# Kernel tuning notes

Hardware: AMD Instinct MI355X
Metric: run time of the kernel (lower is better)

Reference implementation:

```python
import jax, jax.numpy as jnp
import numpy as np

B, D, C, F = 1024, 8192, 345, 512
PROTO_W = 0.99  # args.proto_m


def setup_inputs() -> dict:
    key = jax.random.key(0)
    k = jax.random.split(key, 6)
    img_q = jax.random.normal(k[0], (B, D), jnp.float32)
    img_q1 = jax.random.normal(k[1], (B, D), jnp.float32)
    # partial label mask: random candidate set, guarantee >=1 candidate per row
    partial_Y = (jax.random.uniform(k[2], (B, C)) < 0.3).astype(jnp.float32)
    partial_Y = partial_Y.at[jnp.arange(B), jnp.arange(B) % C].set(1.0)
    W_enc = jax.random.normal(k[3], (D, F), jnp.float32) / np.sqrt(D).astype(np.float32)
    W_fc = jax.random.normal(k[4], (F, C), jnp.float32) / np.sqrt(F).astype(np.float32)
    b_fc = jnp.zeros((C,), jnp.float32)
    proto = jax.random.normal(k[5], (C, F), jnp.float32)
    proto = proto / jnp.linalg.norm(proto, axis=1, keepdims=True)
    return {"img_q": img_q, "img_q1": img_q1, "partial_Y": partial_Y,
            "W_enc": W_enc, "W_fc": W_fc, "b_fc": b_fc, "proto": proto}


def reference(img_q, img_q1, partial_Y, W_enc, W_fc, b_fc, proto):
    # encoder: feats [B,F], logits [B,C] (abstracted backbone + shared fc)
    feats_q = img_q @ W_enc
    logits_q = feats_q @ W_fc + b_fc
    feats_q1 = img_q1 @ W_enc
    logits_q1 = feats_q1 @ W_fc + b_fc

    # partial-label restricted pseudo labels
    scores = jax.nn.softmax(logits_q, axis=1) * partial_Y
    scores = scores / scores.sum(axis=1, keepdims=True)
    labels = jnp.argmax(scores, axis=1)  # [B] int

    # Sequential per-sample EMA p[l] = w*p[l] + (1-w)*f, vectorized in closed form.
    # For a sample with c_after same-label samples occurring later, its final
    # contribution is (1-w)*w^c_after * f; the old prototype is scaled by w^count.
    onehot = jax.nn.one_hot(labels, C, dtype=feats_q.dtype)   # [B,C]
    cum = jnp.cumsum(onehot, axis=0)                          # inclusive counts
    occ = cum[jnp.arange(B), labels] - 1.0                    # occurrences before i
    total = cum[-1]                                           # [C] per-class counts
    c_after = total[labels] - occ - 1.0                       # [B]
    coef = (1.0 - PROTO_W) * PROTO_W ** c_after               # [B]
    contrib = jax.ops.segment_sum(coef[:, None] * feats_q, labels, num_segments=C)
    new_proto = (PROTO_W ** total)[:, None] * proto + contrib
    new_proto = new_proto / jnp.linalg.norm(new_proto, axis=1, keepdims=True)

    prot_scores = new_proto @ W_fc + b_fc
    return logits_q, logits_q1, new_proto, prot_scores, labels, feats_q, feats_q1
```

## Files before the change

### kernel.cpp

```cpp
#include <hip/hip_runtime.h>
#include <float.h>
#include <math.h>

#define B_SZ 1024
#define D_SZ 8192
#define C_SZ 345
#define F_SZ 512
#define PROTO_W 0.99f


#define WS_XH 0
#define WS_XL 33554432u
#define WS_WH 67108864u
#define WS_WL 75497472u
#define WS_P  83886080u
#define WS2_WFH 100663296u
#define WS2_WFL 101056512u
#define WS2_LAB 101449728u
#define WS2_NEED 101457920u
#define WS2_FH 0u
#define WS2_FL 2097152u

#define WS_NEED 92274688u
#define WS_FH  0u
#define WS_FL  2097152u
#define WS_WFH 4194304u
#define WS_WFL 4587520u
#define WS_NPH 4980736u
#define WS_NPL 5373952u

typedef short bf16x8 __attribute__((ext_vector_type(8)));
typedef short short4v __attribute__((ext_vector_type(4)));
typedef short short8v __attribute__((ext_vector_type(8)));
typedef float f32x4  __attribute__((ext_vector_type(4)));

__device__ __forceinline__ void split_bf16(float x, short& hi, short& lo) {
    unsigned u = __float_as_uint(x);
    unsigned r = (u + 0x7FFFu + ((u >> 16) & 1u)) >> 16;
    hi = (short)r;
    float hf = __uint_as_float(r << 16);
    lo = (short)(__float_as_uint(x - hf) >> 16);
}
__device__ __forceinline__ float bf16_f32(short h) {
    return __uint_as_float(((unsigned)(unsigned short)h) << 16);
}

__device__ __forceinline__ void gl_lds16(const short* g, short* l) {
    __builtin_amdgcn_global_load_lds(
        (const __attribute__((address_space(1))) void*)g,
        (__attribute__((address_space(3))) void*)l, 16, 0, 0);
}

__device__ __forceinline__ unsigned f2key(float v) {
    unsigned u = __float_as_uint(v);
    return (u & 0x80000000u) ? ~u : (u | 0x80000000u);
}

__device__ __forceinline__ void fence_barrier() {
    asm volatile("" ::: "memory");
    __builtin_amdgcn_s_barrier();
    asm volatile("" ::: "memory");
}

#define MFMA_BF16 __builtin_amdgcn_mfma_f32_16x16x32_bf16

#define MFMA_BLOCK(IA0, IA1, IB0, IB1)                                   \
    do {                                                                 \
        bf16x8 a0h = *(const bf16x8*)&sAh[IA0];                          \
        bf16x8 a1h = *(const bf16x8*)&sAh[IA1];                          \
        bf16x8 b0h = *(const bf16x8*)&sBh[IB0];                          \
        bf16x8 b1h = *(const bf16x8*)&sBh[IB1];                          \
        bf16x8 a0l = *(const bf16x8*)&sAl[IA0];                          \
        bf16x8 a1l = *(const bf16x8*)&sAl[IA1];                          \
        bf16x8 b0l = *(const bf16x8*)&sBl[IB0];                          \
        bf16x8 b1l = *(const bf16x8*)&sBl[IB1];                          \
        acc[0][0] = MFMA_BF16(a0h, b0h, acc[0][0], 0, 0, 0);             \
        acc[0][1] = MFMA_BF16(a0h, b1h, acc[0][1], 0, 0, 0);             \
        acc[1][0] = MFMA_BF16(a1h, b0h, acc[1][0], 0, 0, 0);             \
        acc[1][1] = MFMA_BF16(a1h, b1h, acc[1][1], 0, 0, 0);             \
        acc[0][0] = MFMA_BF16(a0h, b0l, acc[0][0], 0, 0, 0);             \
        acc[0][1] = MFMA_BF16(a0h, b1l, acc[0][1], 0, 0, 0);             \
        acc[1][0] = MFMA_BF16(a1h, b0l, acc[1][0], 0, 0, 0);             \
        acc[1][1] = MFMA_BF16(a1h, b1l, acc[1][1], 0, 0, 0);             \
        acc[0][0] = MFMA_BF16(a0l, b0h, acc[0][0], 0, 0, 0);             \
        acc[0][1] = MFMA_BF16(a0l, b1h, acc[0][1], 0, 0, 0);             \
        acc[1][0] = MFMA_BF16(a1l, b0h, acc[1][0], 0, 0, 0);             \
        acc[1][1] = MFMA_BF16(a1l, b1h, acc[1][1], 0, 0, 0);             \
    } while (0)

__global__ __launch_bounds__(256) void convert_all(
    const float* __restrict__ img_q, const float* __restrict__ img_q1,
    const float* __restrict__ W_enc, const float* __restrict__ W_fc,
    short* __restrict__ Xh, short* __restrict__ Xl,
    short* __restrict__ Wh, short* __restrict__ Wl,
    short* __restrict__ Wth, short* __restrict__ Wtl)
{
    __shared__ float tile[64][65];
    const int bid = blockIdx.x;
    const int t = threadIdx.x;

    if (bid < 1024) {
        const int HALF = (B_SZ * D_SZ) / 4;
        const int total = 2 * HALF;
        for (int i4 = bid * 256 + t; i4 < total; i4 += 1024 * 256) {
            float4 v = (i4 < HALF) ? ((const float4*)img_q)[i4]
                                   : ((const float4*)img_q1)[i4 - HALF];
            short4v h, l;
            short hh, ll;
            split_bf16(v.x, hh, ll); h.x = hh; l.x = ll;
            split_bf16(v.y, hh, ll); h.y = hh; l.y = ll;
            split_bf16(v.z, hh, ll); h.z = hh; l.z = ll;
            split_bf16(v.w, hh, ll); h.w = hh; l.w = ll;
            ((short4v*)Xh)[i4] = h;
            ((short4v*)Xl)[i4] = l;
        }
    } else if (bid < 2048) {
        const int id = bid - 1024;
        const int k0 = (id >> 3) * 64;
        const int n0 = (id & 7) * 64;
        {
            const int kr = t >> 2;
            const int cb = (t & 3) * 16;
#pragma unroll
            for (int j = 0; j < 4; ++j) {
                float4 v = *(const float4*)&W_enc[(size_t)(k0 + kr) * F_SZ + n0 + cb + j * 4];
                tile[kr][cb + j * 4 + 0] = v.x;
                tile[kr][cb + j * 4 + 1] = v.y;
                tile[kr][cb + j * 4 + 2] = v.z;
                tile[kr][cb + j * 4 + 3] = v.w;
            }
        }
        __syncthreads();
        const int n = t >> 2;
#pragma unroll
        for (int cc = 0; cc < 2; ++cc) {
            const int ch = (t & 3) * 2 + cc;
            short8v h, l;
#pragma unroll
            for (int e = 0; e < 8; ++e) {
                short hh, ll;
                split_bf16(tile[ch * 8 + e][n], hh, ll);
                h[e] = hh; l[e] = ll;
            }
            size_t off = (size_t)(n0 + n) * D_SZ + k0 + ch * 8;
            *(short8v*)&Wh[off] = h;
            *(short8v*)&Wl[off] = l;
        }
    } else {
        const int id = bid - 2048;
        const int k0 = (id & 7) * 64;
        const int c0 = (id >> 3) * 64;
        for (int idx = t; idx < 64 * 64; idx += 256) {
            const int kr = idx >> 6;
            const int cc = idx & 63;
            tile[kr][cc] = (c0 + cc < C_SZ) ? W_fc[(size_t)(k0 + kr) * C_SZ + c0 + cc] : 0.0f;
        }
        __syncthreads();
        const int crow = t >> 2;
#pragma unroll
        for (int cc2 = 0; cc2 < 2; ++cc2) {
            const int ch = (t & 3) * 2 + cc2;
            short8v h, l;
#pragma unroll
            for (int e = 0; e < 8; ++e) {
                short hh, ll;
                split_bf16(tile[ch * 8 + e][crow], hh, ll);
                h[e] = hh; l[e] = ll;
            }
            size_t off = (size_t)(c0 + crow) * F_SZ + k0 + ch * 8;
            *(short8v*)&Wth[off] = h;
            *(short8v*)&Wtl[off] = l;
        }
    }
}

__global__ __launch_bounds__(256, 1) void gemm_ws128(
    const short* __restrict__ Xh, const short* __restrict__ Xl,
    const short* __restrict__ Wh, const short* __restrict__ Wl,
    float* __restrict__ P, int ksteps)
{
    __shared__ __align__(16) short sAh[2][8192];
    __shared__ __align__(16) short sAl[2][8192];
    __shared__ __align__(16) short sBh[2][8192];
    __shared__ __align__(16) short sBl[2][8192];

    const int t = threadIdx.x;
    const int lane = t & 63;
    const int wave = t >> 6;
    const int nt = blockIdx.x;
    const int mt = blockIdx.y;
    const int ks = blockIdx.z;
    const int m0 = mt * 128;
    const int n0 = nt * 128;
    const int kbase = ks * ksteps * 64;

    const short* gbase =
        (wave == 0) ? Xh + (size_t)m0 * D_SZ :
        (wave == 1) ? Xl + (size_t)m0 * D_SZ :
        (wave == 2) ? Wh + (size_t)n0 * D_SZ :
                      Wl + (size_t)n0 * D_SZ;
    short* lb[2];
    lb[0] = (wave == 0) ? sAh[0] : (wave == 1) ? sAl[0] : (wave == 2) ? sBh[0] : sBl[0];
    lb[1] = (wave == 0) ? sAh[1] : (wave == 1) ? sAl[1] : (wave == 2) ? sBh[1] : sBl[1];
    const int lrow8 = lane >> 3;
    const int gchunkOff = ((lane & 7) ^ lrow8) * 8;
    const short* gsrc = gbase + (size_t)lrow8 * D_SZ + kbase + gchunkOff;

    const int mo = (wave >> 1) * 64;
    const int no = (wave & 1) * 64;
    const int lr = lane & 15;
    const int lkg = lane >> 4;
    const int x7 = lr & 7;
    const int sl0 = lkg ^ x7;
    const int sl1 = (4 + lkg) ^ x7;
    int aoff[4], boff[4];
#pragma unroll
    for (int f = 0; f < 4; ++f) {
        aoff[f] = (mo + 16 * f + lr) * 64;
        boff[f] = (no + 16 * f + lr) * 64;
    }

    f32x4 acc[4][4] = {};

#pragma unroll
    for (int j = 0; j < 16; ++j)
        gl_lds16(gsrc + (size_t)(8 * j) * D_SZ, lb[0] + j * 512);

    int buf = 0;
    for (int s = 0; s < ksteps; ++s) {
        if (s + 1 < ksteps) {
            short* dst = lb[buf ^ 1];
            const short* g = gsrc + (s + 1) * 64;
#pragma unroll
            for (int j = 0; j < 16; ++j)
                gl_lds16(g + (size_t)(8 * j) * D_SZ, dst + j * 512);
            asm volatile("s_waitcnt vmcnt(16)" ::: "memory");
        } else {
            asm volatile("s_waitcnt vmcnt(0)" ::: "memory");
        }
        fence_barrier();

        __builtin_amdgcn_s_setprio(1);
        {
            const short* pAh = sAh[buf];
            const short* pAl = sAl[buf];
            const short* pBh = sBh[buf];
            const short* pBl = sBl[buf];
#pragma unroll
            for (int ksub = 0; ksub < 2; ++ksub) {
                const int sl = ksub ? sl1 : sl0;
                bf16x8 ah[4], al[4], bh[4], blo[4];
#pragma unroll
                for (int f = 0; f < 4; ++f) {
                    ah[f]  = *(const bf16x8*)&pAh[aoff[f] + sl * 8];
                    al[f]  = *(const bf16x8*)&pAl[aoff[f] + sl * 8];
                }
#pragma unroll
                for (int g = 0; g < 4; ++g) {
                    bh[g]  = *(const bf16x8*)&pBh[boff[g] + sl * 8];
                    blo[g] = *(const bf16x8*)&pBl[boff[g] + sl * 8];
                }
#pragma unroll
                for (int f = 0; f < 4; ++f)
#pragma unroll
                    for (int g = 0; g < 4; ++g)
                        acc[f][g] = MFMA_BF16(ah[f], bh[g], acc[f][g], 0, 0, 0);
#pragma unroll
                for (int f = 0; f < 4; ++f)
#pragma unroll
                    for (int g = 0; g < 4; ++g)
                        acc[f][g] = MFMA_BF16(ah[f], blo[g], acc[f][g], 0, 0, 0);
#pragma unroll
                for (int f = 0; f < 4; ++f)
#pragma unroll
                    for (int g = 0; g < 4; ++g)
                        acc[f][g] = MFMA_BF16(al[f], bh[g], acc[f][g], 0, 0, 0);
            }
        }
        __builtin_amdgcn_s_setprio(0);
        fence_barrier();
        buf ^= 1;
    }

    float* Pout = P + (size_t)ks * (2048u * 512u);
#pragma unroll
    for (int f = 0; f < 4; ++f)
#pragma unroll
        for (int g = 0; g < 4; ++g) {
            const int col  = n0 + no + 16 * g + (lane & 15);
            const int row0 = m0 + mo + 16 * f + (lane >> 4) * 4;
#pragma unroll
            for (int r = 0; r < 4; ++r)
                Pout[(size_t)(row0 + r) * F_SZ + col] = acc[f][g][r];
        }
}

__global__ __launch_bounds__(256) void reduce_feats4(
    const float* __restrict__ P, float* __restrict__ feats,
    short* __restrict__ Fh, short* __restrict__ Fl)
{
    const int i4 = blockIdx.x * 256 + threadIdx.x;
    float4 a = ((const float4*)P)[i4];
#pragma unroll
    for (int sl = 1; sl < 4; ++sl) {
        float4 b = ((const float4*)(P + (size_t)sl * (2048u * 512u)))[i4];
        a.x += b.x; a.y += b.y; a.z += b.z; a.w += b.w;
    }
    ((float4*)feats)[i4] = a;
    float v[4] = {a.x, a.y, a.z, a.w};
    short4v h, l;
    short hh, ll;
#pragma unroll
    for (int e = 0; e < 4; ++e) {
        split_bf16(v[e], hh, ll); h[e] = hh; l[e] = ll;
    }
    ((short4v*)Fh)[i4] = h;
    ((short4v*)Fl)[i4] = l;
}

__global__ __launch_bounds__(256, 2) void fc_logits3(
    const short* __restrict__ Ah, const short* __restrict__ Al,
    const short* __restrict__ Bh_g, const short* __restrict__ Bl_g,
    const float* __restrict__ bias, const float* __restrict__ partial_Y,
    float* __restrict__ logits, unsigned long long* __restrict__ labPack)
{
    __shared__ __align__(16) short dAh[2][4096];
    __shared__ __align__(16) short dAl[2][4096];
    __shared__ __align__(16) short dBh[2][4096];
    __shared__ __align__(16) short dBl[2][4096];

    const int t = threadIdx.x;
    const int lane = t & 63;
    const int wave = t >> 6;
    const int n0 = blockIdx.x * 64;
    const int m0 = blockIdx.y * 64;

    const int lrow8 = lane >> 3;
    const int colOff = ((lane & 7) ^ lrow8) * 8;

    const short* gsrc = (wave == 0) ? Ah : (wave == 1) ? Al
                      : (wave == 2) ? Bh_g : Bl_g;
    const int rbase = (wave < 2) ? m0 : n0;
    short* lb[2];
    lb[0] = (wave == 0) ? dAh[0] : (wave == 1) ? dAl[0] : (wave == 2) ? dBh[0] : dBl[0];
    lb[1] = (wave == 0) ? dAh[1] : (wave == 1) ? dAl[1] : (wave == 2) ? dBh[1] : dBl[1];
    const short* gbase = gsrc + (size_t)(rbase + lrow8) * F_SZ + colOff;

    const int mo = (wave >> 1) * 32;
    const int no = (wave & 1) * 32;
    const int lr = lane & 15;
    const int lkg = lane >> 4;
    const int x7 = lr & 7;
    const int sl0 = (0 + lkg) ^ x7;
    const int sl1 = (4 + lkg) ^ x7;
    const int ra0 = (mo + lr) * 64,      ra1 = (mo + 16 + lr) * 64;
    const int rb0 = (no + lr) * 64,      rb1 = (no + 16 + lr) * 64;
    const int a00 = ra0 + sl0 * 8, a01 = ra0 + sl1 * 8;
    const int a10 = ra1 + sl0 * 8, a11 = ra1 + sl1 * 8;
    const int b00 = rb0 + sl0 * 8, b01 = rb0 + sl1 * 8;
    const int b10 = rb1 + sl0 * 8, b11 = rb1 + sl1 * 8;

    f32x4 acc[2][2] = {};

#pragma unroll
    for (int j = 0; j < 8; ++j)
        gl_lds16(gbase + (size_t)(8 * j) * F_SZ, lb[0] + j * 512);

    int buf = 0;
    for (int s = 0; s < 8; ++s) {
        if (s + 1 < 8) {
            short* dst = lb[buf ^ 1];
            const short* g = gbase + (s + 1) * 64;
#pragma unroll
            for (int j = 0; j < 8; ++j)
                gl_lds16(g + (size_t)(8 * j) * F_SZ, dst + j * 512);
            asm volatile("s_waitcnt vmcnt(8)" ::: "memory");
        } else {
            asm volatile("s_waitcnt vmcnt(0)" ::: "memory");
        }
        fence_barrier();
        __builtin_amdgcn_s_setprio(1);
        {
            const short* sAh = dAh[buf];
            const short* sAl = dAl[buf];
            const short* sBh = dBh[buf];
            const short* sBl = dBl[buf];
            MFMA_BLOCK(a00, a10, b00, b10);
            MFMA_BLOCK(a01, a11, b01, b11);
        }
        __builtin_amdgcn_s_setprio(0);
        fence_barrier();
        buf ^= 1;
    }

    const bool doArg = (m0 < B_SZ);
#pragma unroll
    for (int f = 0; f < 2; ++f) {
#pragma unroll
        for (int r = 0; r < 4; ++r) {
            const int row = m0 + mo + f * 16 + (lane >> 4) * 4 + r;
            unsigned long long best = 0;
#pragma unroll
            for (int g = 0; g < 2; ++g) {
                const int col = n0 + no + g * 16 + (lane & 15);
                if (col < C_SZ) {
                    const float v = acc[f][g][r] + bias[col];
                    logits[(size_t)row * C_SZ + col] = v;
                    if (doArg && partial_Y[(size_t)row * C_SZ + col] != 0.0f) {
                        unsigned long long p = ((unsigned long long)f2key(v) << 32)
                                             | (unsigned long long)(0xFFFFFFFFu - (unsigned)col);
                        if (p > best) best = p;
                    }
                }
            }
            if (doArg) {
#pragma unroll
                for (int m = 1; m < 16; m <<= 1) {
                    unsigned long long o = __shfl_xor(best, m);
                    if (o > best) best = o;
                }
                if ((lane & 15) == 0 && best != 0)
                    atomicMax(&labPack[row], best);
            }
        }
    }
}

__global__ __launch_bounds__(512) void proto_scores_fused(
    const unsigned long long* __restrict__ labPack,
    const float* __restrict__ feats_q,
    const float* __restrict__ proto,
    const short* __restrict__ Wth, const short* __restrict__ Wtl,
    const float* __restrict__ b_fc,
    float* __restrict__ new_proto, float* __restrict__ scores,
    float* __restrict__ labels_f)
{
    __shared__ int rowlist[B_SZ];
    __shared__ int mcount_s;
    __shared__ float nprow[F_SZ];
    __shared__ float red[8];
    __shared__ float rinv_s;
    const int c = blockIdx.x;
    const int t = threadIdx.x;
    const int lane = t & 63;
    const int w = t >> 6;

    if (c == 0) {
#pragma unroll
        for (int j = 0; j < 2; ++j) {
            const int i = t + j * 512;
            int li = (int)(0xFFFFFFFFu - (unsigned)(labPack[i] & 0xFFFFFFFFull));
            labels_f[i] = (float)li;
        }
    }

    if (w == 0) {
        int k = 0;
#pragma unroll
        for (int ch = 0; ch < 16; ++ch) {
            unsigned long long pk = labPack[ch * 64 + lane];
            int li = (int)(0xFFFFFFFFu - (unsigned)(pk & 0xFFFFFFFFull));
            unsigned long long mask = __ballot(li == c);
            if (lane == 0) {
                while (mask) {
                    int p = __builtin_ctzll(mask);
                    mask &= mask - 1;
                    rowlist[k++] = ch * 64 + p;
                }
            }
            k = __shfl(k, 0);
        }
        if (lane == 0) mcount_s = k;
    }
    __syncthreads();
    const int m = mcount_s;

    float val = proto[(size_t)c * F_SZ + t];
    for (int k = 0; k < m; ++k)
        val = PROTO_W * val + (1.0f - PROTO_W) * feats_q[(size_t)rowlist[k] * F_SZ + t];

    float sq = val * val;
#pragma unroll
    for (int off = 32; off; off >>= 1) sq += __shfl_down(sq, off);
    if ((t & 63) == 0) red[t >> 6] = sq;
    __syncthreads();
    if (t == 0) {
        float s = 0.0f;
#pragma unroll
        for (int ww = 0; ww < 8; ++ww) s += red[ww];
        rinv_s = 1.0f / sqrtf(s);
    }
    __syncthreads();
    const float v = val * rinv_s;
    new_proto[(size_t)c * F_SZ + t] = v;
    nprow[t] = v;
    __syncthreads();

    float np8[8];
#pragma unroll
    for (int j = 0; j < 8; ++j) np8[j] = nprow[lane * 8 + j];
    for (int col = w; col < C_SZ; col += 8) {
        const short8v h = *(const short8v*)&Wth[(size_t)col * F_SZ + lane * 8];
        const short8v l = *(const short8v*)&Wtl[(size_t)col * F_SZ + lane * 8];
        float p = 0.0f;
#pragma unroll
        for (int j = 0; j < 8; ++j)
            p += np8[j] * (bf16_f32(h[j]) + bf16_f32(l[j]));
#pragma unroll
        for (int off = 32; off; off >>= 1) p += __shfl_down(p, off);
        if (lane == 0) scores[(size_t)c * C_SZ + col] = p + b_fc[col];
    }
}

__global__ __launch_bounds__(256) void reduce_feats_split(
    const float* __restrict__ P, float* __restrict__ feats,
    short* __restrict__ Fh, short* __restrict__ Fl,
    const float* __restrict__ W_fc,
    short* __restrict__ Wth, short* __restrict__ Wtl)
{
    const int bid = blockIdx.x;
    const int t = threadIdx.x;
    if (bid < 1024) {
        const int n4 = (2048 * 512) / 4;
        const float* P1 = P + 2048 * 512;
        for (int i4 = bid * 256 + t; i4 < n4; i4 += 1024 * 256) {
            float4 a = ((const float4*)P)[i4];
            float4 b = ((const float4*)P1)[i4];
            float v[4] = {a.x + b.x, a.y + b.y, a.z + b.z, a.w + b.w};
            short4v h, l;
            short hh, ll;
#pragma unroll
            for (int e = 0; e < 4; ++e) {
                feats[i4 * 4 + e] = v[e];
                split_bf16(v[e], hh, ll); h[e] = hh; l[e] = ll;
            }
            ((short4v*)Fh)[i4] = h;
            ((short4v*)Fl)[i4] = l;
        }
    } else {
        __shared__ float tile[64][65];
        const int id = bid - 1024;
        const int k0 = (id & 7) * 64;
        const int c0 = (id >> 3) * 64;
        for (int idx = t; idx < 64 * 64; idx += 256) {
            const int kr = idx >> 6;
            const int cc = idx & 63;
            tile[kr][cc] = (c0 + cc < C_SZ) ? W_fc[(size_t)(k0 + kr) * C_SZ + c0 + cc] : 0.0f;
        }
        __syncthreads();
        const int crow = t >> 2;
#pragma unroll
        for (int cc2 = 0; cc2 < 2; ++cc2) {
            const int ch = (t & 3) * 2 + cc2;
            short8v h, l;
#pragma unroll
            for (int e = 0; e < 8; ++e) {
                short hh, ll;
                split_bf16(tile[ch * 8 + e][crow], hh, ll);
                h[e] = hh; l[e] = ll;
            }
            size_t off = (size_t)(c0 + crow) * F_SZ + k0 + ch * 8;
            *(short8v*)&Wth[off] = h;
            *(short8v*)&Wtl[off] = l;
        }
    }
}

__global__ __launch_bounds__(256) void gemm_fc(
    const short* __restrict__ Ah, const short* __restrict__ Al,
    const short* __restrict__ Bh, const short* __restrict__ Bl,
    const float* __restrict__ bias, float* __restrict__ Cout, int M)
{
    __shared__ __align__(16) short sAh[4096];
    __shared__ __align__(16) short sAl[4096];
    __shared__ __align__(16) short sBh[4096];
    __shared__ __align__(16) short sBl[4096];

    const int t = threadIdx.x;
    const int lane = t & 63;
    const int wave = t >> 6;
    const int n0 = blockIdx.x * 64;
    const int m0 = blockIdx.y * 64;

    const int lrow8 = lane >> 3;
    const int colOff = ((lane & 7) ^ lrow8) * 8;

    short* lbase = (wave == 0) ? sAh : (wave == 1) ? sAl : (wave == 2) ? sBh : sBl;
    const short* gA = (wave == 1) ? Al : Ah;
    const short* gB = (wave == 3) ? Bl : Bh;
    const bool isA = wave < 2;

    const int mo = (wave >> 1) * 32;
    const int no = (wave & 1) * 32;
    const int lr = lane & 15;
    const int lkg = lane >> 4;
    const int x7 = lr & 7;
    const int sl0 = (0 + lkg) ^ x7;
    const int sl1 = (4 + lkg) ^ x7;
    const int ra0 = (mo + lr) * 64,      ra1 = (mo + 16 + lr) * 64;
    const int rb0 = (no + lr) * 64,      rb1 = (no + 16 + lr) * 64;
    const int a00 = ra0 + sl0 * 8, a01 = ra0 + sl1 * 8;
    const int a10 = ra1 + sl0 * 8, a11 = ra1 + sl1 * 8;
    const int b00 = rb0 + sl0 * 8, b01 = rb0 + sl1 * 8;
    const int b10 = rb1 + sl0 * 8, b11 = rb1 + sl1 * 8;

    f32x4 acc[2][2] = {};

    for (int s = 0; s < 8; ++s) {
        __syncthreads();
        if (isA) {
#pragma unroll
            for (int j = 0; j < 8; ++j) {
                int row = m0 + lrow8 + 8 * j;
                if (row > M - 1) row = M - 1;
                gl_lds16(gA + (size_t)row * F_SZ + s * 64 + colOff, lbase + j * 512);
            }
        } else {
#pragma unroll
            for (int j = 0; j < 8; ++j) {
                int row = n0 + lrow8 + 8 * j;
                gl_lds16(gB + (size_t)row * F_SZ + s * 64 + colOff, lbase + j * 512);
            }
        }
        __syncthreads();
        MFMA_BLOCK(a00, a10, b00, b10);
        MFMA_BLOCK(a01, a11, b01, b11);
    }

#pragma unroll
    for (int f = 0; f < 2; ++f)
#pragma unroll
        for (int g = 0; g < 2; ++g) {
            const int col  = n0 + no + g * 16 + (lane & 15);
            if (col >= C_SZ) continue;
            const float bb = bias[col];
            const int row0 = m0 + mo + f * 16 + (lane >> 4) * 4;
#pragma unroll
            for (int r = 0; r < 4; ++r) {
                const int row = row0 + r;
                if (row < M)
                    Cout[(size_t)row * C_SZ + col] = acc[f][g][r] + bb;
            }
        }
}

__global__ __launch_bounds__(64) void argmax_labels(
    const float* __restrict__ logits, const float* __restrict__ partial_Y,
    float* __restrict__ labels_f)
{
    const int i = blockIdx.x;
    const int lane = threadIdx.x;
    float best = -FLT_MAX;
    int bidx = C_SZ;
    for (int c = lane; c < C_SZ; c += 64) {
        if (partial_Y[(size_t)i * C_SZ + c] != 0.0f) {
            float v = logits[(size_t)i * C_SZ + c];
            if (v > best || (v == best && c < bidx)) { best = v; bidx = c; }
        }
    }
#pragma unroll
    for (int off = 32; off; off >>= 1) {
        float ov = __shfl_down(best, off);
        int oi = __shfl_down(bidx, off);
        if (ov > best || (ov == best && oi < bidx)) { best = ov; bidx = oi; }
    }
    if (lane == 0) labels_f[i] = (float)bidx;
}

__global__ __launch_bounds__(512) void proto_update(
    const float* __restrict__ labels_f, const float* __restrict__ feats_q,
    const float* __restrict__ proto, float* __restrict__ new_proto,
    short* __restrict__ NPh, short* __restrict__ NPl)
{
    __shared__ int lab[B_SZ];
    __shared__ float red[8];
    __shared__ float rinv_s;
    const int c = blockIdx.x;
    const int t = threadIdx.x;
    for (int i = t; i < B_SZ; i += 512) lab[i] = (int)labels_f[i];
    __syncthreads();
    float val = proto[(size_t)c * F_SZ + t];
    for (int i = 0; i < B_SZ; ++i) {
        if (lab[i] == c)
            val = PROTO_W * val + (1.0f - PROTO_W) * feats_q[(size_t)i * F_SZ + t];
    }
    float sq = val * val;
#pragma unroll
    for (int off = 32; off; off >>= 1) sq += __shfl_down(sq, off);
    if ((t & 63) == 0) red[t >> 6] = sq;
    __syncthreads();
    if (t == 0) {
        float s = 0.0f;
#pragma unroll
        for (int w = 0; w < 8; ++w) s += red[w];
        rinv_s = 1.0f / sqrtf(s);
    }
    __syncthreads();
    const float v = val * rinv_s;
    new_proto[(size_t)c * F_SZ + t] = v;
    if (NPh) {
        short hh, ll;
        split_bf16(v, hh, ll);
        NPh[(size_t)c * F_SZ + t] = hh;
        NPl[(size_t)c * F_SZ + t] = ll;
    }
}

extern "C" void kernel_launch(void* const* d_in, const int* in_sizes, int n_in,
                              void* d_out, int out_size, void* d_ws, size_t ws_size,
                              hipStream_t stream)
{
    const float* img_q     = (const float*)d_in[0];
    const float* img_q1    = (const float*)d_in[1];
    const float* partial_Y = (const float*)d_in[2];
    const float* W_enc     = (const float*)d_in[3];
    const float* W_fc      = (const float*)d_in[4];
    const float* b_fc      = (const float*)d_in[5];
    const float* proto     = (const float*)d_in[6];

    float* out       = (float*)d_out;
    float* logits    = out;
    float* new_proto = out + 706560;
    float* scores    = out + 883200;
    float* labels_f  = out + 1002225;
    float* feats     = out + 1003249;

    char* ws = (char*)d_ws;
    short* Xh = (short*)(ws + WS_XH);
    short* Xl = (short*)(ws + WS_XL);
    short* Wh = (short*)(ws + WS_WH);
    short* Wl = (short*)(ws + WS_WL);
    float* P  = (float*)(ws + WS_P);

    if (ws_size >= (size_t)WS2_NEED) {
        short* Wth = (short*)(ws + WS2_WFH);
        short* Wtl = (short*)(ws + WS2_WFL);
        unsigned long long* labPack = (unsigned long long*)(ws + WS2_LAB);
        short* Fh = (short*)(ws + WS2_FH);
        short* Fl = (short*)(ws + WS2_FL);

        hipMemsetAsync(labPack, 0, B_SZ * sizeof(unsigned long long), stream);
        hipLaunchKernelGGL(convert_all, dim3(2096), dim3(256), 0, stream,
                           img_q, img_q1, W_enc, W_fc, Xh, Xl, Wh, Wl, Wth, Wtl);
        hipLaunchKernelGGL(gemm_ws128, dim3(4, 16, 4), dim3(256), 0, stream,
                           Xh, Xl, Wh, Wl, P, 32);
        hipLaunchKernelGGL(reduce_feats4, dim3(1024), dim3(256), 0, stream,
                           P, feats, Fh, Fl);
        hipLaunchKernelGGL(fc_logits3, dim3(6, 32), dim3(256), 0, stream,
                           Fh, Fl, Wth, Wtl, b_fc, partial_Y, logits, labPack);
        hipLaunchKernelGGL(proto_scores_fused, dim3(345), dim3(512), 0, stream,
                           labPack, feats, proto, Wth, Wtl, b_fc,
                           new_proto, scores, labels_f);
    } else {
        short* Fh  = (short*)(ws + WS_FH);
        short* Fl  = (short*)(ws + WS_FL);
        short* Wth = (short*)(ws + WS_WFH);
        short* Wtl = (short*)(ws + WS_WFL);
        short* NPh = (short*)(ws + WS_NPH);
        short* NPl = (short*)(ws + WS_NPL);

        hipLaunchKernelGGL(convert_all, dim3(2048), dim3(256), 0, stream,
                           img_q, img_q1, W_enc, W_fc, Xh, Xl, Wh, Wl,
                           (short*)nullptr, (short*)nullptr);
        hipLaunchKernelGGL(gemm_ws128, dim3(4, 16, 2), dim3(256), 0, stream,
                           Xh, Xl, Wh, Wl, P, 64);
        hipLaunchKernelGGL(reduce_feats_split, dim3(1072), dim3(256), 0, stream,
                           P, feats, Fh, Fl, W_fc, Wth, Wtl);
        hipLaunchKernelGGL(gemm_fc, dim3(6, 32), dim3(256), 0, stream,
                           Fh, Fl, Wth, Wtl, b_fc, logits, 2048);
        hipLaunchKernelGGL(argmax_labels, dim3(1024), dim3(64), 0, stream,
                           logits, partial_Y, labels_f);
        hipLaunchKernelGGL(proto_update, dim3(345), dim3(512), 0, stream,
                           labels_f, feats, proto, new_proto, NPh, NPl);
        hipLaunchKernelGGL(gemm_fc, dim3(6, 6), dim3(256), 0, stream,
                           NPh, NPl, Wth, Wtl, b_fc, scores, C_SZ);
    }
}
```

Baseline: 250.1 us.

## Use 512-thread GEMM variant with XCD-aware block remap and per-wave staging

Adds a new split-bf16 GEMM kernel launched with 8 waves per block instead of 4. Each wave owns a 64x32 output sub-tile and loads half of one operand array into LDS with direct global-to-LDS copies. Block indices are permuted so that blocks sharing an XCD work on related tiles, and MFMA sections are raised to high priority. The aim is more latency hiding and better L2 locality, at the cost of more barriers per k-step and more register pressure from the wider block.

```diff
diff --git a/kernel.cpp b/kernel.cpp
--- a/kernel.cpp
+++ b/kernel.cpp
@@ -174,6 +174,163 @@
     }
 }
 
+__global__ __launch_bounds__(512, 1) void gemm_ws128_v3(
+    const short* __restrict__ Xh, const short* __restrict__ Xl,
+    const short* __restrict__ Wh, const short* __restrict__ Wl,
+    float* __restrict__ P, int ksteps)
+{
+    __shared__ __align__(16) short sAh[2][8192];
+    __shared__ __align__(16) short sAl[2][8192];
+    __shared__ __align__(16) short sBh[2][8192];
+    __shared__ __align__(16) short sBl[2][8192];
+
+    const int t = threadIdx.x;
+    const int lane = t & 63;
+    const int wave = t >> 6;
+
+    const int flat = blockIdx.x + 4 * blockIdx.y + 64 * blockIdx.z;
+    const int logical = (flat & 7) * 32 + (flat >> 3);
+    const int nt = logical & 3;
+    const int mt = (logical >> 2) & 15;
+    const int ks = logical >> 6;
+
+    const int m0 = mt * 128;
+    const int n0 = nt * 128;
+    const int kbase = ks * ksteps * 64;
+
+    const int arr = wave >> 1;
+    const int half = wave & 1;
+    const short* gbase =
+        (arr == 0) ? Xh + (size_t)m0 * D_SZ :
+        (arr == 1) ? Xl + (size_t)m0 * D_SZ :
+        (arr == 2) ? Wh + (size_t)n0 * D_SZ :
+                     Wl + (size_t)n0 * D_SZ;
+    short* lb[2];
+    lb[0] = ((arr == 0) ? sAh[0] : (arr == 1) ? sAl[0] : (arr == 2) ? sBh[0] : sBl[0]) + half * 4096;
+    lb[1] = ((arr == 0) ? sAh[1] : (arr == 1) ? sAl[1] : (arr == 2) ? sBh[1] : sBl[1]) + half * 4096;
+    const int lrow8 = lane >> 3;
+    const int gchunkOff = ((lane & 7) ^ lrow8) * 8;
+    const short* gsrc = gbase + (size_t)(half * 64 + lrow8) * D_SZ + kbase + gchunkOff;
+
+    const int wr = wave >> 2;
+    const int wc = wave & 3;
+    const int mo = wr * 64;
+    const int no = wc * 32;
+    const int lr = lane & 15;
+    const int lkg = lane >> 4;
+    const int x7 = lr & 7;
+    const int sl0 = lkg ^ x7;
+    const int sl1 = (4 + lkg) ^ x7;
+    int aoff[4], boff[2];
+#pragma unroll
+    for (int f = 0; f < 4; ++f) aoff[f] = (mo + 16 * f + lr) * 64;
+#pragma unroll
+    for (int g = 0; g < 2; ++g) boff[g] = (no + 16 * g + lr) * 64;
+
+    f32x4 acc[4][2] = {};
+
+#pragma unroll
+    for (int j = 0; j < 8; ++j)
+        gl_lds16(gsrc + (size_t)(8 * j) * D_SZ, lb[0] + j * 512);
+
+    int buf = 0;
+    for (int s = 0; s < ksteps; ++s) {
+        if (s + 1 < ksteps) {
+            short* dst = lb[buf ^ 1];
+            const short* g = gsrc + (s + 1) * 64;
+#pragma unroll
+            for (int j = 0; j < 8; ++j)
+                gl_lds16(g + (size_t)(8 * j) * D_SZ, dst + j * 512);
+            asm volatile("s_waitcnt vmcnt(8)" ::: "memory");
+        } else {
+            asm volatile("s_waitcnt vmcnt(0)" ::: "memory");
+        }
+        fence_barrier();
+
+        const short* pAh = sAh[buf];
+        const short* pAl = sAl[buf];
+        const short* pBh = sBh[buf];
+        const short* pBl = sBl[buf];
+
+        {
+            bf16x8 ah[4], al[4], bh[2], bl_[2];
+#pragma unroll
+            for (int f = 0; f < 4; ++f) {
+                ah[f] = *(const bf16x8*)&pAh[aoff[f] + sl0 * 8];
+                al[f] = *(const bf16x8*)&pAl[aoff[f] + sl0 * 8];
+            }
+#pragma unroll
+            for (int g = 0; g < 2; ++g) {
+                bh[g]  = *(const bf16x8*)&pBh[boff[g] + sl0 * 8];
+                bl_[g] = *(const bf16x8*)&pBl[boff[g] + sl0 * 8];
+            }
+            __builtin_amdgcn_s_setprio(1);
+#pragma unroll
+            for (int f = 0; f < 4; ++f)
+#pragma unroll
+                for (int g = 0; g < 2; ++g)
+                    acc[f][g] = MFMA_BF16(ah[f], bh[g], acc[f][g], 0, 0, 0);
+#pragma unroll
+            for (int f = 0; f < 4; ++f)
+#pragma unroll
+                for (int g = 0; g < 2; ++g)
+                    acc[f][g] = MFMA_BF16(ah[f], bl_[g], acc[f][g], 0, 0, 0);
+#pragma unroll
+            for (int f = 0; f < 4; ++f)
+#pragma unroll
+                for (int g = 0; g < 2; ++g)
+                    acc[f][g] = MFMA_BF16(al[f], bh[g], acc[f][g], 0, 0, 0);
+            __builtin_amdgcn_s_setprio(0);
+        }
+        fence_barrier();
+
+        {
+            bf16x8 ah[4], al[4], bh[2], bl_[2];
+#pragma unroll
+            for (int f = 0; f < 4; ++f) {
+                ah[f] = *(const bf16x8*)&pAh[aoff[f] + sl1 * 8];
+                al[f] = *(const bf16x8*)&pAl[aoff[f] + sl1 * 8];
+            }
+#pragma unroll
+            for (int g = 0; g < 2; ++g) {
+                bh[g]  = *(const bf16x8*)&pBh[boff[g] + sl1 * 8];
+                bl_[g] = *(const bf16x8*)&pBl[boff[g] + sl1 * 8];
+            }
+            __builtin_amdgcn_s_setprio(1);
+#pragma unroll
+            for (int f = 0; f < 4; ++f)
+#pragma unroll
+                for (int g = 0; g < 2; ++g)
+                    acc[f][g] = MFMA_BF16(ah[f], bh[g], acc[f][g], 0, 0, 0);
+#pragma unroll
+            for (int f = 0; f < 4; ++f)
+#pragma unroll
+                for (int g = 0; g < 2; ++g)
+                    acc[f][g] = MFMA_BF16(ah[f], bl_[g], acc[f][g], 0, 0, 0);
+#pragma unroll
+            for (int f = 0; f < 4; ++f)
+#pragma unroll
+                for (int g = 0; g < 2; ++g)
+                    acc[f][g] = MFMA_BF16(al[f], bh[g], acc[f][g], 0, 0, 0);
+            __builtin_amdgcn_s_setprio(0);
+        }
+        fence_barrier();
+        buf ^= 1;
+    }
+
+    float* Pout = P + (size_t)ks * (2048u * 512u);
+#pragma unroll
+    for (int f = 0; f < 4; ++f)
+#pragma unroll
+        for (int g = 0; g < 2; ++g) {
+            const int col  = n0 + no + 16 * g + (lane & 15);
+            const int row0 = m0 + mo + 16 * f + (lane >> 4) * 4;
+#pragma unroll
+            for (int r = 0; r < 4; ++r)
+                Pout[(size_t)(row0 + r) * F_SZ + col] = acc[f][g][r];
+        }
+}
+
 __global__ __launch_bounds__(256, 1) void gemm_ws128(
     const short* __restrict__ Xh, const short* __restrict__ Xl,
     const short* __restrict__ Wh, const short* __restrict__ Wl,
@@ -742,7 +899,7 @@
         hipMemsetAsync(labPack, 0, B_SZ * sizeof(unsigned long long), stream);
         hipLaunchKernelGGL(convert_all, dim3(2096), dim3(256), 0, stream,
                            img_q, img_q1, W_enc, W_fc, Xh, Xl, Wh, Wl, Wth, Wtl);
-        hipLaunchKernelGGL(gemm_ws128, dim3(4, 16, 4), dim3(256), 0, stream,
+        hipLaunchKernelGGL(gemm_ws128_v3, dim3(4, 16, 4), dim3(512), 0, stream,
                            Xh, Xl, Wh, Wl, P, 32);
         hipLaunchKernelGGL(reduce_feats4, dim3(1024), dim3(256), 0, stream,
                            P, feats, Fh, Fl);
```

Result: no change. 248.2 us (-0.8%).
